# Kernel optimization log

Hardware: AMD Instinct MI355X
Metric: run time of the kernel (lower is better)

## Reference

```python
import jax, jax.numpy as jnp
import numpy as np

N, E, G = 100000, 1600000, 64
IN_DIM, EMB, HID, HEADS, OUT = 128, 128, 32, 4, 64
CAT = HID * HEADS  # 128
EPS = 1e-5
SLOPE = 0.2


def gat_conv(x, src, dst, W, a_src, a_dst, bias):
    # x: [N, F_in]; W: [HEADS*HID, F_in]; a_*: [1, HEADS, HID]; bias: [HEADS*HID]
    h = (x @ W.T).reshape(N, HEADS, HID)
    s_src = (h * a_src).sum(-1)  # [N, HEADS]
    s_dst = (h * a_dst).sum(-1)
    e = jax.nn.leaky_relu(s_src[src] + s_dst[dst], SLOPE)  # [Etot, HEADS]
    m = jax.ops.segment_max(e, dst, num_segments=N)
    p = jnp.exp(e - m[dst])
    denom = jax.ops.segment_sum(p, dst, num_segments=N)
    alpha = p / denom[dst]  # softmax over incoming edges per dst node
    out = jax.ops.segment_sum(h[src] * alpha[:, :, None], dst, num_segments=N)
    return out.reshape(N, CAT) + bias


def graph_norm(x, batch, w, b, mean_scale):
    cnt = jax.ops.segment_sum(jnp.ones((N,), x.dtype), batch, num_segments=G)[:, None]
    mean = jax.ops.segment_sum(x, batch, num_segments=G) / cnt  # [G, C]
    sub = x - mean_scale * mean[batch]
    var = jax.ops.segment_sum(sub * sub, batch, num_segments=G) / cnt
    inv = 1.0 / jnp.sqrt(var + EPS)
    return w * sub * inv[batch] + b


def setup_inputs() -> dict:
    key = jax.random.key(0)
    ks = jax.random.split(key, 20)
    g = lambda k, shape, s: jax.random.normal(k, shape, dtype=jnp.float32) * s
    inp = {
        'x': g(ks[0], (N, IN_DIM), 1.0),
        'edge_index': jax.random.randint(ks[1], (2, E), 0, N, dtype=jnp.int64 if jax.config.read('jax_enable_x64') else jnp.int32),
        'batch': jnp.sort(jax.random.randint(ks[2], (N,), 0, G)),
        'enc_w': g(ks[3], (EMB, IN_DIM), 0.08),
        'enc_b': jnp.zeros((EMB,), jnp.float32),
        'w1': g(ks[4], (HEADS * HID, EMB), 0.08),
        'att_src1': g(ks[5], (1, HEADS, HID), 0.15),
        'att_dst1': g(ks[6], (1, HEADS, HID), 0.15),
        'b1': jnp.zeros((CAT,), jnp.float32),
        'n1_w': jnp.ones((CAT,), jnp.float32),
        'n1_b': jnp.zeros((CAT,), jnp.float32),
        'n1_ms': jnp.ones((CAT,), jnp.float32),
        'w2': g(ks[7], (HEADS * HID, CAT), 0.08),
        'att_src2': g(ks[8], (1, HEADS, HID), 0.15),
        'att_dst2': g(ks[9], (1, HEADS, HID), 0.15),
        'b2': jnp.zeros((CAT,), jnp.float32),
        'n2_w': jnp.ones((CAT,), jnp.float32),
        'n2_b': jnp.zeros((CAT,), jnp.float32),
        'n2_ms': jnp.ones((CAT,), jnp.float32),
        'fc_w': g(ks[10], (OUT, CAT), 0.08),
        'fc_b': jnp.zeros((OUT,), jnp.float32),
    }
    return inp


def reference(x, edge_index, batch, enc_w, enc_b, w1, att_src1, att_dst1, b1,
              n1_w, n1_b, n1_ms, w2, att_src2, att_dst2, b2, n2_w, n2_b, n2_ms,
              fc_w, fc_b):
    # PyG GATConv adds self-loops by default
    loops = jnp.arange(N, dtype=edge_index.dtype)
    src = jnp.concatenate([edge_index[0], loops])
    dst = jnp.concatenate([edge_index[1], loops])

    h = x @ enc_w.T + enc_b
    h = jax.nn.elu(gat_conv(h, src, dst, w1, att_src1, att_dst1, b1))
    h = graph_norm(h, batch, n1_w, n1_b, n1_ms)  # dropout = identity (eval)
    h = jax.nn.elu(gat_conv(h, src, dst, w2, att_src2, att_dst2, b2))
    h = graph_norm(h, batch, n2_w, n2_b, n2_ms)
    pooled = jax.ops.segment_max(h, batch, num_segments=G)  # global_max_pool
    return pooled @ fc_w.T + fc_b  # out_dim != 1 -> no sigmoid
```

## Files before the change

### kernel.cpp

```cpp
#include <hip/hip_runtime.h>
#include <hip/hip_bf16.h>

#define SLOPE 0.2f
#define EPS_GN 1e-5f
#define APITCH 136
#define NBUCK 391

typedef __attribute__((ext_vector_type(8))) short bfrag;
typedef __attribute__((ext_vector_type(4))) float ffrag;

__device__ __forceinline__ float lrelu(float v) { return v > 0.f ? v : SLOPE * v; }
__device__ __forceinline__ unsigned int flipf(float x) {
    unsigned int u = __float_as_uint(x);
    return (u & 0x80000000u) ? ~u : (u | 0x80000000u);
}
__device__ __forceinline__ float unflipf(unsigned int u) {
    return __uint_as_float((u & 0x80000000u) ? (u & 0x7fffffffu) : ~u);
}
__device__ __forceinline__ short f2bs(float v) {
    __hip_bfloat16 h = __float2bfloat16(v);
    return *reinterpret_cast<short*>(&h);
}
__device__ __forceinline__ float blo(unsigned int u) { return __uint_as_float(u << 16); }
__device__ __forceinline__ float bhi(unsigned int u) { return __uint_as_float(u & 0xffff0000u); }

__global__ void zero_kernel(float* __restrict__ p, int n) {
    int i = blockIdx.x * 256 + threadIdx.x;
    if (i < n) p[i] = 0.f;
}

__global__ void prep_weights(const float* __restrict__ enc_w,
                             const float* __restrict__ enc_b,
                             const float* __restrict__ w1,
                             const float* __restrict__ w2,
                             unsigned short* __restrict__ WT1b,
                             unsigned short* __restrict__ WT2b,
                             float* __restrict__ bc1, float* __restrict__ bc2) {
    int c = blockIdx.x;
    int k = threadIdx.x;
    __shared__ float w1row[128];
    w1row[k] = w1[c * 128 + k];
    __syncthreads();
    float acc = 0.f;
    for (int j = 0; j < 128; ++j)
        acc = fmaf(w1row[j], enc_w[j * 128 + k], acc);
    WT1b[c * 128 + k] = (unsigned short)f2bs(acc);
    WT2b[c * 128 + k] = (unsigned short)f2bs(w2[c * 128 + k]);
    if (k == 0) {
        float b = 0.f;
        for (int j = 0; j < 128; ++j) b += w1row[j] * enc_b[j];
        bc1[c] = b;
        bc2[c] = 0.f;
    }
}


__global__ void __launch_bounds__(256) bucket_hist(const int* __restrict__ ei,
                                                   int* __restrict__ bhist, int E, int N) {
    __shared__ int h[NBUCK];
    for (int i = threadIdx.x; i < NBUCK; i += 256) h[i] = 0;
    __syncthreads();
    int base = blockIdx.x * 4096;
#pragma unroll
    for (int s = 0; s < 16; ++s) {
        int e = base + s * 256 + threadIdx.x;
        if (e < E + N) {
            int dst = (e < E) ? ei[E + e] : (e - E);
            atomicAdd(&h[dst >> 8], 1);
        }
    }
    __syncthreads();
    for (int i = threadIdx.x; i < NBUCK; i += 256)
        if (h[i]) atomicAdd(&bhist[i], h[i]);
}

__global__ void bucket_scan(const int* __restrict__ bhist,
                            int* __restrict__ bbase, int* __restrict__ bcur) {
    __shared__ int sh[512];
    int t = threadIdx.x;
    int v = (t < NBUCK) ? bhist[t] : 0;
    sh[t] = v;
    __syncthreads();
    for (int off = 1; off < 512; off <<= 1) {
        int add = (t >= off) ? sh[t - off] : 0;
        __syncthreads();
        sh[t] += add;
        __syncthreads();
    }
    if (t < NBUCK) {
        bbase[t] = sh[t] - v;
        bcur[t] = sh[t] - v;
    }
}

__global__ void __launch_bounds__(256) bucket_scatter(const int* __restrict__ ei,
                                                      int* __restrict__ bcur,
                                                      unsigned int* __restrict__ staging,
                                                      int E, int N) {
    __shared__ int h[NBUCK];
    __shared__ int lb[NBUCK];
    for (int i = threadIdx.x; i < NBUCK; i += 256) h[i] = 0;
    __syncthreads();
    int base = blockIdx.x * 4096;
    int srcv[16], dstv[16];
#pragma unroll
    for (int s = 0; s < 16; ++s) {
        int e = base + s * 256 + threadIdx.x;
        srcv[s] = -1;
        if (e < E + N) {
            srcv[s] = (e < E) ? ei[e] : (e - E);
            dstv[s] = (e < E) ? ei[E + e] : (e - E);
            atomicAdd(&h[dstv[s] >> 8], 1);
        }
    }
    __syncthreads();
    for (int i = threadIdx.x; i < NBUCK; i += 256) {
        int c = h[i];
        lb[i] = c ? atomicAdd(&bcur[i], c) : 0;
        h[i] = 0;
    }
    __syncthreads();
#pragma unroll
    for (int s = 0; s < 16; ++s) {
        if (srcv[s] >= 0) {
            int b = dstv[s] >> 8;
            int slot = atomicAdd(&h[b], 1);
            staging[lb[b] + slot] = ((unsigned int)srcv[s] << 8) | (unsigned int)(dstv[s] & 255);
        }
    }
}

__global__ void __launch_bounds__(256) bucket_finalize(
    const unsigned int* __restrict__ staging,
    const int* __restrict__ bbase, const int* __restrict__ bcur,
    int* __restrict__ rowp, int* __restrict__ esrc, int N, int Etot) {
    int b = blockIdx.x, t = threadIdx.x;
    __shared__ int h[256], sc[256];
    h[t] = 0;
    __syncthreads();
    int s0 = bbase[b], s1 = bcur[b];
    for (int j = s0 + t; j < s1; j += 256)
        atomicAdd(&h[staging[j] & 255], 1);
    __syncthreads();
    int d = h[t];
    sc[t] = d;
    __syncthreads();
    for (int off = 1; off < 256; off <<= 1) {
        int add = (t >= off) ? sc[t - off] : 0;
        __syncthreads();
        sc[t] += add;
        __syncthreads();
    }
    int excl = s0 + sc[t] - d;
    int node = b * 256 + t;
    if (node < N) rowp[node] = excl;
    if (b == 0 && t == 0) rowp[N] = Etot;
    __syncthreads();
    h[t] = excl;
    __syncthreads();
    for (int j = s0 + t; j < s1; j += 256) {
        unsigned int p = staging[j];
        int pos = atomicAdd(&h[p & 255], 1);
        esrc[pos] = (int)(p >> 8);
    }
}

__global__ void __launch_bounds__(256) gemm_mfma(
    const void* __restrict__ Ain, const unsigned short* __restrict__ WTb,
    const float* __restrict__ bias, const float* __restrict__ att_src,
    const float* __restrict__ att_dst, const int* __restrict__ batch,
    const float* __restrict__ Ac, const float* __restrict__ Bc,
    unsigned int* __restrict__ H, float* __restrict__ ssrc, float* __restrict__ sdst, int N) {
    __shared__ short Bsh[128 * APITCH];
    __shared__ short Ash[64 * APITCH];
    __shared__ float asrc_s[128], adst_s[128], bias_s[128];
    int tid = threadIdx.x;
    int base = blockIdx.x * 64;

    for (int idx = tid; idx < 2048; idx += 256) {
        int c = idx >> 4, k8 = (idx & 15) * 8;
        uint4 wv = ((const uint4*)WTb)[idx];
        *(uint4*)&Bsh[c * APITCH + k8] = wv;
    }
    if (Ac == nullptr) {
        const float* A = (const float*)Ain;
        for (int idx = tid; idx < 2048; idx += 256) {
            int nl = idx >> 5, k4 = (idx & 31) * 4;
            int node = base + nl;
            float4 v = make_float4(0.f, 0.f, 0.f, 0.f);
            if (node < N) v = ((const float4*)A)[node * 32 + (idx & 31)];
            *(short4*)&Ash[nl * APITCH + k4] =
                make_short4(f2bs(v.x), f2bs(v.y), f2bs(v.z), f2bs(v.w));
        }
    } else {
        const uint4* A4 = (const uint4*)Ain;
        for (int idx = tid; idx < 1024; idx += 256) {
            int nl = idx >> 4, u4 = idx & 15, k8 = u4 * 8;
            int node = base + nl;
            short o[8] = {0, 0, 0, 0, 0, 0, 0, 0};
            if (node < N) {
                uint4 hb = A4[node * 16 + u4];
                int g = batch[node];
                float4 a0 = *(const float4*)&Ac[g * 128 + k8];
                float4 a1 = *(const float4*)&Ac[g * 128 + k8 + 4];
                float4 b0 = *(const float4*)&Bc[g * 128 + k8];
                float4 b1 = *(const float4*)&Bc[g * 128 + k8 + 4];
                o[0] = f2bs(fmaf(blo(hb.x), a0.x, b0.x));
                o[1] = f2bs(fmaf(bhi(hb.x), a0.y, b0.y));
                o[2] = f2bs(fmaf(blo(hb.y), a0.z, b0.z));
                o[3] = f2bs(fmaf(bhi(hb.y), a0.w, b0.w));
                o[4] = f2bs(fmaf(blo(hb.z), a1.x, b1.x));
                o[5] = f2bs(fmaf(bhi(hb.z), a1.y, b1.y));
                o[6] = f2bs(fmaf(blo(hb.w), a1.z, b1.z));
                o[7] = f2bs(fmaf(bhi(hb.w), a1.w, b1.w));
            }
            *(bfrag*)&Ash[nl * APITCH + k8] = *(bfrag*)o;
        }
    }
    if (tid < 128) {
        asrc_s[tid] = att_src[tid];
        adst_s[tid] = att_dst[tid];
        bias_s[tid] = bias[tid];
    }
    __syncthreads();

    int w = tid >> 6, lane = tid & 63, col = lane & 15, quad = lane >> 4;
    int rowBase = w * 16;

    bfrag afr[4];
#pragma unroll
    for (int s = 0; s < 4; ++s)
        afr[s] = *(const bfrag*)&Ash[(rowBase + col) * APITCH + s * 32 + quad * 8];

    ffrag acc[8];
#pragma unroll
    for (int t = 0; t < 8; ++t) acc[t] = (ffrag){0.f, 0.f, 0.f, 0.f};

#pragma unroll
    for (int t = 0; t < 8; ++t) {
#pragma unroll
        for (int s = 0; s < 4; ++s) {
            bfrag bfr = *(const bfrag*)&Bsh[(t * 16 + col) * APITCH + s * 32 + quad * 8];
            acc[t] = __builtin_amdgcn_mfma_f32_16x16x32_bf16(afr[s], bfr, acc[t], 0, 0, 0);
        }
    }

#pragma unroll
    for (int t = 0; t < 8; ++t) {
        int ch = t * 16 + col;
        float bv = bias_s[ch];
#pragma unroll
        for (int r = 0; r < 4; ++r)
            Ash[(rowBase + quad * 4 + r) * APITCH + ch] = f2bs(acc[t][r] + bv);
    }
    __syncthreads();

    float2 av = make_float2(asrc_s[lane * 2], asrc_s[lane * 2 + 1]);
    float2 dv = make_float2(adst_s[lane * 2], adst_s[lane * 2 + 1]);
    for (int r = 0; r < 16; ++r) {
        int node = base + rowBase + r;
        unsigned int hb = *(const unsigned int*)&Ash[(rowBase + r) * APITCH + lane * 2];
        float hx = blo(hb);
        float hy = bhi(hb);
        float vs = hx * av.x + hy * av.y;
        float vd = hx * dv.x + hy * dv.y;
#pragma unroll
        for (int off = 8; off; off >>= 1) {
            vs += __shfl_xor(vs, off, 16);
            vd += __shfl_xor(vd, off, 16);
        }
        if (node < N) {
            H[node * 64 + lane] = hb;
            if ((lane & 15) == 0) {
                int h = lane >> 4;
                ssrc[node * 4 + h] = vs;
                sdst[node * 4 + h] = vd;
            }
        }
    }
}

template <int POOL>
__global__ void __launch_bounds__(256) agg_kernel(
    const int* __restrict__ row, const int* __restrict__ esrc,
    const float* __restrict__ ssrc, const float* __restrict__ sdst,
    const uint4* __restrict__ H4, const float* __restrict__ bias,
    uint4* __restrict__ out, const int* __restrict__ batch,
    float* __restrict__ gsum, float* __restrict__ gsq, int* __restrict__ gcnt,
    int countFlag, unsigned int* __restrict__ rawmax,
    unsigned int* __restrict__ rawmin, int N) {
    __shared__ float Ls[4][2][128], Lq[4][2][128];
    __shared__ float Lmx[4][2][128], Lmn[4][2][128];
    __shared__ int cnt2[2];
    int tid = threadIdx.x, w = tid >> 6, lane = tid & 63;
    int slot = lane >> 4, li = lane & 15, head = li >> 2;
    int base = blockIdx.x * 64;
    int g0 = batch[base];
    int g1 = batch[min(base + 63, N - 1)];
    if (tid < 2) cnt2[tid] = 0;
    int c0 = li * 8;
    float bv[8];
#pragma unroll
    for (int p = 0; p < 8; ++p) bv[p] = bias[c0 + p];

    if (slot == 0) {
#pragma unroll
        for (int p = 0; p < 8; ++p) {
            Ls[w][0][c0 + p] = 0.f; Ls[w][1][c0 + p] = 0.f;
            Lq[w][0][c0 + p] = 0.f; Lq[w][1][c0 + p] = 0.f;
            if (POOL) {
                Lmx[w][0][c0 + p] = -3e38f; Lmx[w][1][c0 + p] = -3e38f;
                Lmn[w][0][c0 + p] =  3e38f; Lmn[w][1][c0 + p] =  3e38f;
            }
        }
    }

    float sAcc[8] = {}, qAcc[8] = {};
    float mxA[8], mnA[8];
#pragma unroll
    for (int p = 0; p < 8; ++p) { mxA[p] = -3e38f; mnA[p] = 3e38f; }
    int curSet = 0;

    for (int j = 0; j < 16; ++j) {
        int n = base + w * 16 + j;
        if (n >= N) break;
        int beg = row[n], end = row[n + 1];
        float sdh = sdst[n * 4 + head];
        float num[8] = {0.f, 0.f, 0.f, 0.f, 0.f, 0.f, 0.f, 0.f};
        float den = 0.f;
        for (int e = beg + slot; e < end; e += 4) {
            int s = esrc[e];
            float al = __expf(lrelu(ssrc[s * 4 + head] + sdh));
            uint4 hb = H4[s * 16 + li];
            den += al;
            num[0] = fmaf(al, blo(hb.x), num[0]);
            num[1] = fmaf(al, bhi(hb.x), num[1]);
            num[2] = fmaf(al, blo(hb.y), num[2]);
            num[3] = fmaf(al, bhi(hb.y), num[3]);
            num[4] = fmaf(al, blo(hb.z), num[4]);
            num[5] = fmaf(al, bhi(hb.z), num[5]);
            num[6] = fmaf(al, blo(hb.w), num[6]);
            num[7] = fmaf(al, bhi(hb.w), num[7]);
        }
        den += __shfl_xor(den, 16);
        den += __shfl_xor(den, 32);
#pragma unroll
        for (int p = 0; p < 8; ++p) {
            num[p] += __shfl_xor(num[p], 16);
            num[p] += __shfl_xor(num[p], 32);
        }
        if (slot == 0) {
            int bset = (batch[n] != g0) ? 1 : 0;
            if (bset != curSet) {
#pragma unroll
                for (int p = 0; p < 8; ++p) {
                    Ls[w][curSet][c0 + p] += sAcc[p];
                    Lq[w][curSet][c0 + p] += qAcc[p];
                    sAcc[p] = 0.f; qAcc[p] = 0.f;
                    if (POOL) {
                        Lmx[w][curSet][c0 + p] = fmaxf(Lmx[w][curSet][c0 + p], mxA[p]);
                        Lmn[w][curSet][c0 + p] = fminf(Lmn[w][curSet][c0 + p], mnA[p]);
                        mxA[p] = -3e38f; mnA[p] = 3e38f;
                    }
                }
                curSet = bset;
            }
            float rh = 1.f / den;
            unsigned int o4[4];
#pragma unroll
            for (int p = 0; p < 4; ++p) {
                float v0 = fmaf(num[2 * p], rh, bv[2 * p]);
                float v1 = fmaf(num[2 * p + 1], rh, bv[2 * p + 1]);
                v0 = v0 > 0.f ? v0 : __expf(v0) - 1.f;
                v1 = v1 > 0.f ? v1 : __expf(v1) - 1.f;
                sAcc[2 * p] += v0; qAcc[2 * p] += v0 * v0;
                sAcc[2 * p + 1] += v1; qAcc[2 * p + 1] += v1 * v1;
                if (POOL) {
                    mxA[2 * p] = fmaxf(mxA[2 * p], v0);
                    mnA[2 * p] = fminf(mnA[2 * p], v0);
                    mxA[2 * p + 1] = fmaxf(mxA[2 * p + 1], v1);
                    mnA[2 * p + 1] = fminf(mnA[2 * p + 1], v1);
                }
                o4[p] = ((unsigned int)(unsigned short)f2bs(v0)) |
                        (((unsigned int)(unsigned short)f2bs(v1)) << 16);
            }
            out[n * 16 + li] = make_uint4(o4[0], o4[1], o4[2], o4[3]);
        }
    }
    if (slot == 0) {
#pragma unroll
        for (int p = 0; p < 8; ++p) {
            Ls[w][curSet][c0 + p] += sAcc[p];
            Lq[w][curSet][c0 + p] += qAcc[p];
            if (POOL) {
                Lmx[w][curSet][c0 + p] = fmaxf(Lmx[w][curSet][c0 + p], mxA[p]);
                Lmn[w][curSet][c0 + p] = fminf(Lmn[w][curSet][c0 + p], mnA[p]);
            }
        }
    }
    __syncthreads();
    if (countFlag && tid < 64) {
        int n = base + tid;
        if (n < N) atomicAdd(&cnt2[(batch[n] != g0) ? 1 : 0], 1);
    }
    if (tid < 128) {
        float s0 = Ls[0][0][tid] + Ls[1][0][tid] + Ls[2][0][tid] + Ls[3][0][tid];
        float q0 = Lq[0][0][tid] + Lq[1][0][tid] + Lq[2][0][tid] + Lq[3][0][tid];
        atomicAdd(&gsum[g0 * 128 + tid], s0);
        atomicAdd(&gsq[g0 * 128 + tid], q0);
        if (POOL) {
            float m0 = fmaxf(fmaxf(Lmx[0][0][tid], Lmx[1][0][tid]),
                             fmaxf(Lmx[2][0][tid], Lmx[3][0][tid]));
            float n0 = fminf(fminf(Lmn[0][0][tid], Lmn[1][0][tid]),
                             fminf(Lmn[2][0][tid], Lmn[3][0][tid]));
            if (m0 > -2e38f) atomicMax(&rawmax[g0 * 128 + tid], flipf(m0));
            if (n0 < 2e38f) atomicMin(&rawmin[g0 * 128 + tid], flipf(n0));
        }
        if (g1 != g0) {
            float s1 = Ls[0][1][tid] + Ls[1][1][tid] + Ls[2][1][tid] + Ls[3][1][tid];
            float q1 = Lq[0][1][tid] + Lq[1][1][tid] + Lq[2][1][tid] + Lq[3][1][tid];
            atomicAdd(&gsum[g1 * 128 + tid], s1);
            atomicAdd(&gsq[g1 * 128 + tid], q1);
            if (POOL) {
                float m1 = fmaxf(fmaxf(Lmx[0][1][tid], Lmx[1][1][tid]),
                                 fmaxf(Lmx[2][1][tid], Lmx[3][1][tid]));
                float n1 = fminf(fminf(Lmn[0][1][tid], Lmn[1][1][tid]),
                                 fminf(Lmn[2][1][tid], Lmn[3][1][tid]));
                if (m1 > -2e38f) atomicMax(&rawmax[g1 * 128 + tid], flipf(m1));
                if (n1 < 2e38f) atomicMin(&rawmin[g1 * 128 + tid], flipf(n1));
            }
        }
    }
    __syncthreads();
    if (countFlag && tid < 2) {
        int g = (tid == 0) ? g0 : g1;
        if ((tid == 0 || g1 != g0) && cnt2[tid]) atomicAdd(&gcnt[g], cnt2[tid]);
    }
}

__global__ void norm_coef(const float* __restrict__ gsum, const float* __restrict__ gsq,
                          const int* __restrict__ gcnt,
                          const float* __restrict__ w, const float* __restrict__ b,
                          const float* __restrict__ ms,
                          float* __restrict__ Ac, float* __restrict__ Bc) {
    int g = blockIdx.x, c = threadIdx.x;
    int i = g * 128 + c;
    float cntv = (float)gcnt[g];
    if (cntv < 0.5f) { Ac[i] = 0.f; Bc[i] = 0.f; return; }
    float mean = gsum[i] / cntv;
    float msv = ms[c];
    float var = gsq[i] / cntv - msv * (2.f - msv) * mean * mean;
    var = fmaxf(var, 0.f);
    float inv = rsqrtf(var + EPS_GN);
    float wv = w[c];
    Ac[i] = wv * inv;
    Bc[i] = b[c] - msv * mean * wv * inv;
}

__global__ void fc_kernel(const unsigned int* __restrict__ rawmax,
                          const unsigned int* __restrict__ rawmin,
                          const float* __restrict__ Ac, const float* __restrict__ Bc,
                          const float* __restrict__ fcw,
                          const float* __restrict__ fcb,
                          float* __restrict__ out) {
    int g = blockIdx.x, o = threadIdx.x;
    __shared__ float p[128];
#pragma unroll
    for (int h = 0; h < 2; ++h) {
        int c = o + h * 64;
        float a = Ac[g * 128 + c], bb = Bc[g * 128 + c];
        float M = unflipf(rawmax[g * 128 + c]);
        float m = unflipf(rawmin[g * 128 + c]);
        p[c] = (a >= 0.f) ? fmaf(a, M, bb) : fmaf(a, m, bb);
    }
    __syncthreads();
    float acc = fcb[o];
    for (int k = 0; k < 128; ++k)
        acc = fmaf(p[k], fcw[o * 128 + k], acc);
    out[g * 64 + o] = acc;
}

extern "C" void kernel_launch(void* const* d_in, const int* in_sizes, int n_in,
                              void* d_out, int out_size, void* d_ws, size_t ws_size,
                              hipStream_t stream) {
    const float* x     = (const float*)d_in[0];
    const int* ei      = (const int*)d_in[1];
    const int* batch   = (const int*)d_in[2];
    const float* enc_w = (const float*)d_in[3];
    const float* enc_b = (const float*)d_in[4];
    const float* w1    = (const float*)d_in[5];
    const float* as1   = (const float*)d_in[6];
    const float* ad1   = (const float*)d_in[7];
    const float* b1    = (const float*)d_in[8];
    const float* n1w   = (const float*)d_in[9];
    const float* n1b   = (const float*)d_in[10];
    const float* n1ms  = (const float*)d_in[11];
    const float* w2    = (const float*)d_in[12];
    const float* as2   = (const float*)d_in[13];
    const float* ad2   = (const float*)d_in[14];
    const float* b2    = (const float*)d_in[15];
    const float* n2w   = (const float*)d_in[16];
    const float* n2b   = (const float*)d_in[17];
    const float* n2ms  = (const float*)d_in[18];
    const float* fcw   = (const float*)d_in[19];
    const float* fcb   = (const float*)d_in[20];
    float* out = (float*)d_out;

    int N = in_sizes[2];
    int E = in_sizes[1] / 2;
    int Etot = E + N;

    char* ws = (char*)d_ws;
    size_t off = 0;
    auto take = [&](size_t bytes) {
        char* p = ws + off;
        off = (off + bytes + 255) & ~(size_t)255;
        return p;
    };
    unsigned short* WT1b = (unsigned short*)take(128 * 128 * 2);
    unsigned short* WT2b = (unsigned short*)take(128 * 128 * 2);
    float* bc1 = (float*)take(512);
    float* bc2 = (float*)take(512);
    float* ssrc = (float*)take((size_t)N * 16);
    float* sdst = (float*)take((size_t)N * 16);
    int* rowp   = (int*)take((size_t)(N + 1) * 4);
    int* esrc   = (int*)take((size_t)Etot * 4);
    unsigned int* staging = (unsigned int*)take((size_t)Etot * 4);
    int* bbase  = (int*)take(512 * 4);
    int* bcur   = (int*)take(512 * 4);
    unsigned int* H = (unsigned int*)take((size_t)N * 256);
    unsigned int* AG = (unsigned int*)take((size_t)N * 256);
    float* Ac   = (float*)take(64 * 128 * 4);
    float* Bc   = (float*)take(64 * 128 * 4);
    unsigned int* rawmin = (unsigned int*)take(64 * 128 * 4);
    size_t zbeg = off;
    int* bhist   = (int*)take(512 * 4);
    float* gsumA = (float*)take(64 * 128 * 4);
    float* gsqA  = (float*)take(64 * 128 * 4);
    float* gsumB = (float*)take(64 * 128 * 4);
    float* gsqB  = (float*)take(64 * 128 * 4);
    int* gcnt    = (int*)take(256);
    unsigned int* rawmax = (unsigned int*)take(64 * 128 * 4);
    size_t zend = off;
    if (off > ws_size) return;

    int zn = (int)((zend - zbeg) / 4);
    int EB = (Etot + 4095) / 4096;

    zero_kernel<<<(zn + 255) / 256, 256, 0, stream>>>((float*)(ws + zbeg), zn);
    hipMemsetAsync(rawmin, 0xFF, 64 * 128 * 4, stream);
    prep_weights<<<128, 128, 0, stream>>>(enc_w, enc_b, w1, w2, WT1b, WT2b, bc1, bc2);

    bucket_hist<<<EB, 256, 0, stream>>>(ei, bhist, E, N);
    bucket_scan<<<1, 512, 0, stream>>>(bhist, bbase, bcur);
    bucket_scatter<<<EB, 256, 0, stream>>>(ei, bcur, staging, E, N);
    bucket_finalize<<<NBUCK, 256, 0, stream>>>(staging, bbase, bcur, rowp, esrc, N, Etot);

    gemm_mfma<<<(N + 63) / 64, 256, 0, stream>>>(x, WT1b, bc1, as1, ad1, batch,
                                                 nullptr, nullptr, H, ssrc, sdst, N);
    agg_kernel<0><<<(N + 63) / 64, 256, 0, stream>>>(
        rowp, esrc, ssrc, sdst, (const uint4*)H, b1, (uint4*)AG, batch,
        gsumA, gsqA, gcnt, 1, nullptr, nullptr, N);
    norm_coef<<<64, 128, 0, stream>>>(gsumA, gsqA, gcnt, n1w, n1b, n1ms, Ac, Bc);

    gemm_mfma<<<(N + 63) / 64, 256, 0, stream>>>(AG, WT2b, bc2, as2, ad2, batch,
                                                 Ac, Bc, H, ssrc, sdst, N);
    agg_kernel<1><<<(N + 63) / 64, 256, 0, stream>>>(
        rowp, esrc, ssrc, sdst, (const uint4*)H, b2, (uint4*)AG, batch,
        gsumB, gsqB, gcnt, 0, rawmax, rawmin, N);
    norm_coef<<<64, 128, 0, stream>>>(gsumB, gsqB, gcnt, n2w, n2b, n2ms, Ac, Bc);

    fc_kernel<<<64, 64, 0, stream>>>(rawmax, rawmin, Ac, Bc, fcw, fcb, out);
}
```

Before: 533.7 us.

## Split aggregation from graph-norm stats into separate one-node-per-wave kernels

The aggregation kernel now gives each wave a single destination node and launches N/4 blocks, where before each wave walked 16 nodes in sequence. The per-graph sum, sum-of-squares and max/min statistics move into a separate stats_kernel that re-reads the bf16 output. Per-graph node counts are now found by binary search over the sorted batch array in norm_coef. The zero init and the 0xFF memset are merged into one init kernel. This aims for better load balance and latency hiding in the gather loop, at the cost of an extra pass over the N x 128 bf16 activations and an extra launch per layer.

```diff
diff --git a/kernel.cpp b/kernel.cpp
--- a/kernel.cpp
+++ b/kernel.cpp
@@ -24,9 +24,10 @@
 __device__ __forceinline__ float blo(unsigned int u) { return __uint_as_float(u << 16); }
 __device__ __forceinline__ float bhi(unsigned int u) { return __uint_as_float(u & 0xffff0000u); }
 
-__global__ void zero_kernel(float* __restrict__ p, int n) {
+__global__ void init_kernel(unsigned int* __restrict__ p, int nzero, int nff) {
     int i = blockIdx.x * 256 + threadIdx.x;
-    if (i < n) p[i] = 0.f;
+    if (i < nzero) p[i] = 0u;
+    else if (i < nzero + nff) p[i] = 0xFFFFFFFFu;
 }
 
 __global__ void prep_weights(const float* __restrict__ enc_w,
@@ -280,172 +281,169 @@
     }
 }
 
-template <int POOL>
 __global__ void __launch_bounds__(256) agg_kernel(
     const int* __restrict__ row, const int* __restrict__ esrc,
     const float* __restrict__ ssrc, const float* __restrict__ sdst,
     const uint4* __restrict__ H4, const float* __restrict__ bias,
-    uint4* __restrict__ out, const int* __restrict__ batch,
-    float* __restrict__ gsum, float* __restrict__ gsq, int* __restrict__ gcnt,
-    int countFlag, unsigned int* __restrict__ rawmax,
-    unsigned int* __restrict__ rawmin, int N) {
-    __shared__ float Ls[4][2][128], Lq[4][2][128];
-    __shared__ float Lmx[4][2][128], Lmn[4][2][128];
-    __shared__ int cnt2[2];
-    int tid = threadIdx.x, w = tid >> 6, lane = tid & 63;
+    uint4* __restrict__ out, int N) {
+    int n = (blockIdx.x * 256 + threadIdx.x) >> 6;
+    int lane = threadIdx.x & 63;
+    if (n >= N) return;
     int slot = lane >> 4, li = lane & 15, head = li >> 2;
+    int beg = row[n], end = row[n + 1];
+    float sdh = sdst[n * 4 + head];
+
+    float num[8] = {0.f, 0.f, 0.f, 0.f, 0.f, 0.f, 0.f, 0.f};
+    float den = 0.f;
+    for (int e = beg + slot; e < end; e += 4) {
+        int s = esrc[e];
+        float al = __expf(lrelu(ssrc[s * 4 + head] + sdh));
+        uint4 hb = H4[s * 16 + li];
+        den += al;
+        num[0] = fmaf(al, blo(hb.x), num[0]);
+        num[1] = fmaf(al, bhi(hb.x), num[1]);
+        num[2] = fmaf(al, blo(hb.y), num[2]);
+        num[3] = fmaf(al, bhi(hb.y), num[3]);
+        num[4] = fmaf(al, blo(hb.z), num[4]);
+        num[5] = fmaf(al, bhi(hb.z), num[5]);
+        num[6] = fmaf(al, blo(hb.w), num[6]);
+        num[7] = fmaf(al, bhi(hb.w), num[7]);
+    }
+    den += __shfl_xor(den, 16);
+    den += __shfl_xor(den, 32);
+#pragma unroll
+    for (int j = 0; j < 8; ++j) {
+        num[j] += __shfl_xor(num[j], 16);
+        num[j] += __shfl_xor(num[j], 32);
+    }
+    if (slot == 0) {
+        float rh = 1.f / den;
+        int c0 = li * 8;
+        unsigned int o[4];
+#pragma unroll
+        for (int p = 0; p < 4; ++p) {
+            float v0 = fmaf(num[2 * p], rh, bias[c0 + 2 * p]);
+            float v1 = fmaf(num[2 * p + 1], rh, bias[c0 + 2 * p + 1]);
+            v0 = v0 > 0.f ? v0 : __expf(v0) - 1.f;
+            v1 = v1 > 0.f ? v1 : __expf(v1) - 1.f;
+            o[p] = ((unsigned int)(unsigned short)f2bs(v0)) |
+                   (((unsigned int)(unsigned short)f2bs(v1)) << 16);
+        }
+        out[n * 16 + li] = make_uint4(o[0], o[1], o[2], o[3]);
+    }
+}
+
+template <int POOL>
+__global__ void __launch_bounds__(256) stats_kernel(
+    const uint4* __restrict__ X4, const int* __restrict__ batch,
+    float* __restrict__ gsum, float* __restrict__ gsq,
+    unsigned int* __restrict__ rawmax, unsigned int* __restrict__ rawmin, int N) {
+    __shared__ float red[16][16][9];
+    int t = threadIdx.x, u4 = t & 15, rg = t >> 4;
     int base = blockIdx.x * 64;
     int g0 = batch[base];
     int g1 = batch[min(base + 63, N - 1)];
-    if (tid < 2) cnt2[tid] = 0;
-    int c0 = li * 8;
-    float bv[8];
-#pragma unroll
-    for (int p = 0; p < 8; ++p) bv[p] = bias[c0 + p];
-
-    if (slot == 0) {
-#pragma unroll
-        for (int p = 0; p < 8; ++p) {
-            Ls[w][0][c0 + p] = 0.f; Ls[w][1][c0 + p] = 0.f;
-            Lq[w][0][c0 + p] = 0.f; Lq[w][1][c0 + p] = 0.f;
+
+    float s[2][8] = {}, q[2][8] = {};
+    float mx[2][8], mn[2][8];
+#pragma unroll
+    for (int st = 0; st < 2; ++st)
+#pragma unroll
+        for (int p = 0; p < 8; ++p) { mx[st][p] = -3e38f; mn[st][p] = 3e38f; }
+
+#pragma unroll
+    for (int rr = 0; rr < 4; ++rr) {
+        int node = base + rg + rr * 16;
+        if (node < N) {
+            uint4 hb = X4[node * 16 + u4];
+            int st = (batch[node] != g0) ? 1 : 0;
+            float vv[8] = {blo(hb.x), bhi(hb.x), blo(hb.y), bhi(hb.y),
+                           blo(hb.z), bhi(hb.z), blo(hb.w), bhi(hb.w)};
+#pragma unroll
+            for (int p = 0; p < 8; ++p) {
+                s[st][p] += vv[p];
+                q[st][p] += vv[p] * vv[p];
+                if (POOL) {
+                    mx[st][p] = fmaxf(mx[st][p], vv[p]);
+                    mn[st][p] = fminf(mn[st][p], vv[p]);
+                }
+            }
+        }
+    }
+
+    int c = t, uu = t >> 3, ch = t & 7;
+    float rs[2], rq[2], rmx[2], rmn[2];
+    int nset = (g1 != g0) ? 2 : 1;
+    for (int st = 0; st < nset; ++st) {
+#pragma unroll
+        for (int p = 0; p < 8; ++p) red[rg][u4][p] = s[st][p];
+        __syncthreads();
+        if (t < 128) {
+            float a = 0.f;
+            for (int r2 = 0; r2 < 16; ++r2) a += red[r2][uu][ch];
+            rs[st] = a;
+        }
+        __syncthreads();
+#pragma unroll
+        for (int p = 0; p < 8; ++p) red[rg][u4][p] = q[st][p];
+        __syncthreads();
+        if (t < 128) {
+            float a = 0.f;
+            for (int r2 = 0; r2 < 16; ++r2) a += red[r2][uu][ch];
+            rq[st] = a;
+        }
+        __syncthreads();
+        if (POOL) {
+#pragma unroll
+            for (int p = 0; p < 8; ++p) red[rg][u4][p] = mx[st][p];
+            __syncthreads();
+            if (t < 128) {
+                float a = -3e38f;
+                for (int r2 = 0; r2 < 16; ++r2) a = fmaxf(a, red[r2][uu][ch]);
+                rmx[st] = a;
+            }
+            __syncthreads();
+#pragma unroll
+            for (int p = 0; p < 8; ++p) red[rg][u4][p] = mn[st][p];
+            __syncthreads();
+            if (t < 128) {
+                float a = 3e38f;
+                for (int r2 = 0; r2 < 16; ++r2) a = fminf(a, red[r2][uu][ch]);
+                rmn[st] = a;
+            }
+            __syncthreads();
+        }
+    }
+    if (t < 128) {
+        for (int st = 0; st < nset; ++st) {
+            int g = (st == 0) ? g0 : g1;
+            atomicAdd(&gsum[g * 128 + c], rs[st]);
+            atomicAdd(&gsq[g * 128 + c], rq[st]);
             if (POOL) {
-                Lmx[w][0][c0 + p] = -3e38f; Lmx[w][1][c0 + p] = -3e38f;
-                Lmn[w][0][c0 + p] =  3e38f; Lmn[w][1][c0 + p] =  3e38f;
+                if (rmx[st] > -2e38f) atomicMax(&rawmax[g * 128 + c], flipf(rmx[st]));
+                if (rmn[st] < 2e38f) atomicMin(&rawmin[g * 128 + c], flipf(rmn[st]));
             }
         }
     }
-
-    float sAcc[8] = {}, qAcc[8] = {};
-    float mxA[8], mnA[8];
-#pragma unroll
-    for (int p = 0; p < 8; ++p) { mxA[p] = -3e38f; mnA[p] = 3e38f; }
-    int curSet = 0;
-
-    for (int j = 0; j < 16; ++j) {
-        int n = base + w * 16 + j;
-        if (n >= N) break;
-        int beg = row[n], end = row[n + 1];
-        float sdh = sdst[n * 4 + head];
-        float num[8] = {0.f, 0.f, 0.f, 0.f, 0.f, 0.f, 0.f, 0.f};
-        float den = 0.f;
-        for (int e = beg + slot; e < end; e += 4) {
-            int s = esrc[e];
-            float al = __expf(lrelu(ssrc[s * 4 + head] + sdh));
-            uint4 hb = H4[s * 16 + li];
-            den += al;
-            num[0] = fmaf(al, blo(hb.x), num[0]);
-            num[1] = fmaf(al, bhi(hb.x), num[1]);
-            num[2] = fmaf(al, blo(hb.y), num[2]);
-            num[3] = fmaf(al, bhi(hb.y), num[3]);
-            num[4] = fmaf(al, blo(hb.z), num[4]);
-            num[5] = fmaf(al, bhi(hb.z), num[5]);
-            num[6] = fmaf(al, blo(hb.w), num[6]);
-            num[7] = fmaf(al, bhi(hb.w), num[7]);
-        }
-        den += __shfl_xor(den, 16);
-        den += __shfl_xor(den, 32);
-#pragma unroll
-        for (int p = 0; p < 8; ++p) {
-            num[p] += __shfl_xor(num[p], 16);
-            num[p] += __shfl_xor(num[p], 32);
-        }
-        if (slot == 0) {
-            int bset = (batch[n] != g0) ? 1 : 0;
-            if (bset != curSet) {
-#pragma unroll
-                for (int p = 0; p < 8; ++p) {
-                    Ls[w][curSet][c0 + p] += sAcc[p];
-                    Lq[w][curSet][c0 + p] += qAcc[p];
-                    sAcc[p] = 0.f; qAcc[p] = 0.f;
-                    if (POOL) {
-                        Lmx[w][curSet][c0 + p] = fmaxf(Lmx[w][curSet][c0 + p], mxA[p]);
-                        Lmn[w][curSet][c0 + p] = fminf(Lmn[w][curSet][c0 + p], mnA[p]);
-                        mxA[p] = -3e38f; mnA[p] = 3e38f;
-                    }
-                }
-                curSet = bset;
-            }
-            float rh = 1.f / den;
-            unsigned int o4[4];
-#pragma unroll
-            for (int p = 0; p < 4; ++p) {
-                float v0 = fmaf(num[2 * p], rh, bv[2 * p]);
-                float v1 = fmaf(num[2 * p + 1], rh, bv[2 * p + 1]);
-                v0 = v0 > 0.f ? v0 : __expf(v0) - 1.f;
-                v1 = v1 > 0.f ? v1 : __expf(v1) - 1.f;
-                sAcc[2 * p] += v0; qAcc[2 * p] += v0 * v0;
-                sAcc[2 * p + 1] += v1; qAcc[2 * p + 1] += v1 * v1;
-                if (POOL) {
-                    mxA[2 * p] = fmaxf(mxA[2 * p], v0);
-                    mnA[2 * p] = fminf(mnA[2 * p], v0);
-                    mxA[2 * p + 1] = fmaxf(mxA[2 * p + 1], v1);
-                    mnA[2 * p + 1] = fminf(mnA[2 * p + 1], v1);
-                }
-                o4[p] = ((unsigned int)(unsigned short)f2bs(v0)) |
-                        (((unsigned int)(unsigned short)f2bs(v1)) << 16);
-            }
-            out[n * 16 + li] = make_uint4(o4[0], o4[1], o4[2], o4[3]);
-        }
-    }
-    if (slot == 0) {
-#pragma unroll
-        for (int p = 0; p < 8; ++p) {
-            Ls[w][curSet][c0 + p] += sAcc[p];
-            Lq[w][curSet][c0 + p] += qAcc[p];
-            if (POOL) {
-                Lmx[w][curSet][c0 + p] = fmaxf(Lmx[w][curSet][c0 + p], mxA[p]);
-                Lmn[w][curSet][c0 + p] = fminf(Lmn[w][curSet][c0 + p], mnA[p]);
-            }
-        }
-    }
-    __syncthreads();
-    if (countFlag && tid < 64) {
-        int n = base + tid;
-        if (n < N) atomicAdd(&cnt2[(batch[n] != g0) ? 1 : 0], 1);
-    }
-    if (tid < 128) {
-        float s0 = Ls[0][0][tid] + Ls[1][0][tid] + Ls[2][0][tid] + Ls[3][0][tid];
-        float q0 = Lq[0][0][tid] + Lq[1][0][tid] + Lq[2][0][tid] + Lq[3][0][tid];
-        atomicAdd(&gsum[g0 * 128 + tid], s0);
-        atomicAdd(&gsq[g0 * 128 + tid], q0);
-        if (POOL) {
-            float m0 = fmaxf(fmaxf(Lmx[0][0][tid], Lmx[1][0][tid]),
-                             fmaxf(Lmx[2][0][tid], Lmx[3][0][tid]));
-            float n0 = fminf(fminf(Lmn[0][0][tid], Lmn[1][0][tid]),
-                             fminf(Lmn[2][0][tid], Lmn[3][0][tid]));
-            if (m0 > -2e38f) atomicMax(&rawmax[g0 * 128 + tid], flipf(m0));
-            if (n0 < 2e38f) atomicMin(&rawmin[g0 * 128 + tid], flipf(n0));
-        }
-        if (g1 != g0) {
-            float s1 = Ls[0][1][tid] + Ls[1][1][tid] + Ls[2][1][tid] + Ls[3][1][tid];
-            float q1 = Lq[0][1][tid] + Lq[1][1][tid] + Lq[2][1][tid] + Lq[3][1][tid];
-            atomicAdd(&gsum[g1 * 128 + tid], s1);
-            atomicAdd(&gsq[g1 * 128 + tid], q1);
-            if (POOL) {
-                float m1 = fmaxf(fmaxf(Lmx[0][1][tid], Lmx[1][1][tid]),
-                                 fmaxf(Lmx[2][1][tid], Lmx[3][1][tid]));
-                float n1 = fminf(fminf(Lmn[0][1][tid], Lmn[1][1][tid]),
-                                 fminf(Lmn[2][1][tid], Lmn[3][1][tid]));
-                if (m1 > -2e38f) atomicMax(&rawmax[g1 * 128 + tid], flipf(m1));
-                if (n1 < 2e38f) atomicMin(&rawmin[g1 * 128 + tid], flipf(n1));
-            }
-        }
-    }
-    __syncthreads();
-    if (countFlag && tid < 2) {
-        int g = (tid == 0) ? g0 : g1;
-        if ((tid == 0 || g1 != g0) && cnt2[tid]) atomicAdd(&gcnt[g], cnt2[tid]);
-    }
 }
 
 __global__ void norm_coef(const float* __restrict__ gsum, const float* __restrict__ gsq,
-                          const int* __restrict__ gcnt,
+                          const int* __restrict__ batch, int N,
                           const float* __restrict__ w, const float* __restrict__ b,
                           const float* __restrict__ ms,
                           float* __restrict__ Ac, float* __restrict__ Bc) {
+    __shared__ float cnt_s;
     int g = blockIdx.x, c = threadIdx.x;
+    if (c == 0) {
+        int lo = 0, hi = N;
+        while (lo < hi) { int m = (lo + hi) >> 1; if (batch[m] < g) lo = m + 1; else hi = m; }
+        int lo2 = lo, hi2 = N;
+        while (lo2 < hi2) { int m = (lo2 + hi2) >> 1; if (batch[m] < g + 1) lo2 = m + 1; else hi2 = m; }
+        cnt_s = (float)(lo2 - lo);
+    }
+    __syncthreads();
     int i = g * 128 + c;
-    float cntv = (float)gcnt[g];
+    float cntv = cnt_s;
     if (cntv < 0.5f) { Ac[i] = 0.f; Bc[i] = 0.f; return; }
     float mean = gsum[i] / cntv;
     float msv = ms[c];
@@ -532,23 +530,25 @@
     unsigned int* AG = (unsigned int*)take((size_t)N * 256);
     float* Ac   = (float*)take(64 * 128 * 4);
     float* Bc   = (float*)take(64 * 128 * 4);
-    unsigned int* rawmin = (unsigned int*)take(64 * 128 * 4);
     size_t zbeg = off;
     int* bhist   = (int*)take(512 * 4);
     float* gsumA = (float*)take(64 * 128 * 4);
     float* gsqA  = (float*)take(64 * 128 * 4);
     float* gsumB = (float*)take(64 * 128 * 4);
     float* gsqB  = (float*)take(64 * 128 * 4);
-    int* gcnt    = (int*)take(256);
     unsigned int* rawmax = (unsigned int*)take(64 * 128 * 4);
     size_t zend = off;
+    unsigned int* rawmin = (unsigned int*)take(64 * 128 * 4);
+    size_t fend = off;
     if (off > ws_size) return;
 
-    int zn = (int)((zend - zbeg) / 4);
+    int nzero = (int)((zend - zbeg) / 4);
+    int nff = (int)((fend - zend) / 4);
     int EB = (Etot + 4095) / 4096;
-
-    zero_kernel<<<(zn + 255) / 256, 256, 0, stream>>>((float*)(ws + zbeg), zn);
-    hipMemsetAsync(rawmin, 0xFF, 64 * 128 * 4, stream);
+    int SB = (N + 63) / 64;
+
+    init_kernel<<<(nzero + nff + 255) / 256, 256, 0, stream>>>(
+        (unsigned int*)(ws + zbeg), nzero, nff);
     prep_weights<<<128, 128, 0, stream>>>(enc_w, enc_b, w1, w2, WT1b, WT2b, bc1, bc2);
 
     bucket_hist<<<EB, 256, 0, stream>>>(ei, bhist, E, N);
@@ -558,17 +558,19 @@
 
     gemm_mfma<<<(N + 63) / 64, 256, 0, stream>>>(x, WT1b, bc1, as1, ad1, batch,
                                                  nullptr, nullptr, H, ssrc, sdst, N);
-    agg_kernel<0><<<(N + 63) / 64, 256, 0, stream>>>(
-        rowp, esrc, ssrc, sdst, (const uint4*)H, b1, (uint4*)AG, batch,
-        gsumA, gsqA, gcnt, 1, nullptr, nullptr, N);
-    norm_coef<<<64, 128, 0, stream>>>(gsumA, gsqA, gcnt, n1w, n1b, n1ms, Ac, Bc);
+    agg_kernel<<<(N + 3) / 4, 256, 0, stream>>>(rowp, esrc, ssrc, sdst,
+                                                (const uint4*)H, b1, (uint4*)AG, N);
+    stats_kernel<0><<<SB, 256, 0, stream>>>((const uint4*)AG, batch, gsumA, gsqA,
+                                            nullptr, nullptr, N);
+    norm_coef<<<64, 128, 0, stream>>>(gsumA, gsqA, batch, N, n1w, n1b, n1ms, Ac, Bc);
 
     gemm_mfma<<<(N + 63) / 64, 256, 0, stream>>>(AG, WT2b, bc2, as2, ad2, batch,
                                                  Ac, Bc, H, ssrc, sdst, N);
-    agg_kernel<1><<<(N + 63) / 64, 256, 0, stream>>>(
-        rowp, esrc, ssrc, sdst, (const uint4*)H, b2, (uint4*)AG, batch,
-        gsumB, gsqB, gcnt, 0, rawmax, rawmin, N);
-    norm_coef<<<64, 128, 0, stream>>>(gsumB, gsqB, gcnt, n2w, n2b, n2ms, Ac, Bc);
+    agg_kernel<<<(N + 3) / 4, 256, 0, stream>>>(rowp, esrc, ssrc, sdst,
+                                                (const uint4*)H, b2, (uint4*)AG, N);
+    stats_kernel<1><<<SB, 256, 0, stream>>>((const uint4*)AG, batch, gsumB, gsqB,
+                                            rawmax, rawmin, N);
+    norm_coef<<<64, 128, 0, stream>>>(gsumB, gsqB, batch, N, n2w, n2b, n2ms, Ac, Bc);
 
     fc_kernel<<<64, 64, 0, stream>>>(rawmax, rawmin, Ac, Bc, fcw, fcb, out);
 }
```

Measured after the change: 564.4 us. 1.06x slower.
